# Optimization experiments

Measured on AMD Instinct MI355X. Metric: run time of the kernel, lower is better.

Reference implementation:

```python
import jax, jax.numpy as jnp
import numpy as np

N_NODES = 100000
N_EDGES = 6400000
D = 12

def setup_inputs() -> dict:
    key = jax.random.key(0)
    k1, k2, k3, k4 = jax.random.split(key, 4)
    x = jax.random.normal(k1, (N_NODES, D), dtype=jnp.float32)
    W_l = jax.random.normal(k2, (D, D), dtype=jnp.float32) / np.sqrt(D)
    W_r = jax.random.normal(k3, (D, D), dtype=jnp.float32) / np.sqrt(D)
    b = jnp.zeros((D,), dtype=jnp.float32)
    edge_index = jax.random.randint(k4, (2, N_EDGES), 0, N_NODES, dtype=jnp.int64)
    return {"x": x, "W_l": W_l, "W_r": W_r, "b": b, "edge_index": edge_index}

def reference(x, W_l, W_r, b, edge_index):
    # PyG SAGEConv (mean aggregation): out = lin_l(mean_{j in N(i)} x_j) + lin_r(x_i)
    src = edge_index[0]
    dst = edge_index[1]
    n = x.shape[0]
    msgs = x[src]                                      # [E, D] gather
    agg = jax.ops.segment_sum(msgs, dst, num_segments=n)          # [N, D]
    cnt = jax.ops.segment_sum(jnp.ones_like(dst, dtype=x.dtype), dst, num_segments=n)
    mean = agg / jnp.maximum(cnt, 1.0)[:, None]        # [N, D]
    out = mean @ W_l.T + x @ W_r.T + b                 # lin_l carries the bias in PyG
    return out
```

## Files before the change

kernel.cpp:

```cpp
#include <hip/hip_runtime.h>

#define N_NODES 100000
#define N_EDGES 6400000
#define D 12

#define SLOG 7
#define SSZ  128
#define NB   ((N_NODES + SSZ - 1) / SSZ)
#define NBLK 512
#define EPB  ((N_EDGES + NBLK - 1) / NBLK)
#define SBLK 256
#define STHR 512
#define SEPB ((N_EDGES + SBLK - 1) / SBLK)
#define RSTR 13

#define CAP  2048
#define EPT  (CAP / 256)

__device__ __forceinline__ unsigned int f2bf(float f) {
    unsigned int u = __float_as_uint(f);
    return (u + 0x7fffu + ((u >> 16) & 1u)) >> 16;
}
__device__ __forceinline__ unsigned int pk2(float lo, float hi) {
    return (f2bf(hi) << 16) | f2bf(lo);
}
__device__ __forceinline__ float bflo(unsigned int u) { return __uint_as_float(u << 16); }
__device__ __forceinline__ float bfhi(unsigned int u) { return __uint_as_float(u & 0xffff0000u); }

__global__ __launch_bounds__(256) void prep_kernel(
    const float* __restrict__ x, unsigned int* __restrict__ xb)
{
    int i = blockIdx.x * 256 + threadIdx.x;
    if (i >= N_NODES) return;
    const float4* xr = (const float4*)(x) + (size_t)i * 3;
    float4 a = xr[0], b = xr[1], c = xr[2];
    unsigned int* o = xb + (size_t)i * 8;
    ((uint4*)o)[0] = make_uint4(pk2(a.x, a.y), pk2(a.z, a.w), pk2(b.x, b.y), pk2(b.z, b.w));
    ((uint2*)(o + 4))[0] = make_uint2(pk2(c.x, c.y), pk2(c.z, c.w));
}

__global__ __launch_bounds__(256) void hist_kernel(
    const int* __restrict__ ei, int* __restrict__ bins)
{
    __shared__ int h[NB];
    for (int i = threadIdx.x; i < NB; i += 256) h[i] = 0;
    __syncthreads();
    const int* dei = ei + N_EDGES;
    int start = blockIdx.x * EPB;
    int end = min(start + EPB, N_EDGES);
    int e = start + (int)threadIdx.x;
    while (e + 768 < end) {
        int d0 = dei[e], d1 = dei[e + 256], d2 = dei[e + 512], d3 = dei[e + 768];
        atomicAdd(&h[d0 >> SLOG], 1);
        atomicAdd(&h[d1 >> SLOG], 1);
        atomicAdd(&h[d2 >> SLOG], 1);
        atomicAdd(&h[d3 >> SLOG], 1);
        e += 1024;
    }
    while (e < end) { atomicAdd(&h[dei[e] >> SLOG], 1); e += 256; }
    __syncthreads();
    for (int i = threadIdx.x; i < NB; i += 256) {
        int c = h[i];
        if (c) atomicAdd(&bins[i], c);
    }
}

__global__ __launch_bounds__(1024) void scan_kernel(
    const int* __restrict__ bins, int* __restrict__ base, int* __restrict__ cursor)
{
    __shared__ int buf[1024];
    __shared__ int carry;
    int tid = threadIdx.x;
    if (tid == 0) carry = 0;
    __syncthreads();
    for (int c0 = 0; c0 < NB; c0 += 1024) {
        int i = c0 + tid;
        int v = (i < NB) ? bins[i] : 0;
        buf[tid] = v;
        __syncthreads();
        for (int o = 1; o < 1024; o <<= 1) {
            int t = (tid >= o) ? buf[tid - o] : 0;
            __syncthreads();
            buf[tid] += t;
            __syncthreads();
        }
        int excl = buf[tid] - v + carry;
        if (i < NB) { base[i] = excl; cursor[i] = excl; }
        __syncthreads();
        if (tid == 0) carry += buf[1023];
        __syncthreads();
    }
    if (tid == 0) base[NB] = N_EDGES;
}

__global__ __launch_bounds__(512) void scatter_sort_kernel(
    const int* __restrict__ ei, int* __restrict__ cursor,
    unsigned int* __restrict__ sorted)
{
    __shared__ int h[NB];
    for (int i = threadIdx.x; i < NB; i += STHR) h[i] = 0;
    __syncthreads();
    const int* dei = ei + N_EDGES;
    int start = blockIdx.x * SEPB;
    int end = min(start + SEPB, N_EDGES);
    int e = start + (int)threadIdx.x;
    while (e + 3 * STHR < end) {
        int d0 = dei[e], d1 = dei[e + STHR], d2 = dei[e + 2 * STHR], d3 = dei[e + 3 * STHR];
        atomicAdd(&h[d0 >> SLOG], 1);
        atomicAdd(&h[d1 >> SLOG], 1);
        atomicAdd(&h[d2 >> SLOG], 1);
        atomicAdd(&h[d3 >> SLOG], 1);
        e += 4 * STHR;
    }
    while (e < end) { atomicAdd(&h[dei[e] >> SLOG], 1); e += STHR; }
    __syncthreads();
    for (int i = threadIdx.x; i < NB; i += STHR) {
        int c = h[i];
        h[i] = c ? atomicAdd(&cursor[i], c) : 0;
    }
    __syncthreads();
    e = start + (int)threadIdx.x;
    while (e + 3 * STHR < end) {
        int s0 = ei[e], s1 = ei[e + STHR], s2 = ei[e + 2 * STHR], s3 = ei[e + 3 * STHR];
        int d0 = dei[e], d1 = dei[e + STHR], d2 = dei[e + 2 * STHR], d3 = dei[e + 3 * STHR];
        int p0 = atomicAdd(&h[d0 >> SLOG], 1);
        int p1 = atomicAdd(&h[d1 >> SLOG], 1);
        int p2 = atomicAdd(&h[d2 >> SLOG], 1);
        int p3 = atomicAdd(&h[d3 >> SLOG], 1);
        sorted[p0] = ((unsigned)s0 << SLOG) | (unsigned)(d0 & (SSZ - 1));
        sorted[p1] = ((unsigned)s1 << SLOG) | (unsigned)(d1 & (SSZ - 1));
        sorted[p2] = ((unsigned)s2 << SLOG) | (unsigned)(d2 & (SSZ - 1));
        sorted[p3] = ((unsigned)s3 << SLOG) | (unsigned)(d3 & (SSZ - 1));
        e += 4 * STHR;
    }
    while (e < end) {
        int s = ei[e], d = dei[e];
        int pos = atomicAdd(&h[d >> SLOG], 1);
        sorted[pos] = ((unsigned)s << SLOG) | (unsigned)(d & (SSZ - 1));
        e += STHR;
    }
}

__global__ __launch_bounds__(256) void agg_reg_kernel(
    const unsigned int* __restrict__ sorted, const int* __restrict__ base,
    const unsigned int* __restrict__ xb,
    const float* __restrict__ x, const float* __restrict__ Wl,
    const float* __restrict__ Wr, const float* __restrict__ bias,
    float* __restrict__ out)
{
    __shared__ float sWl[D * D], sWr[D * D], sb[D];
    __shared__ int cnt[SSZ];
    __shared__ int sbuf[SSZ];
    __shared__ int segbase[SSZ + 1];
    __shared__ int cursor[SSZ];
    __shared__ int cnt_tot[SSZ];
    __shared__ unsigned vals[CAP * 6];

    int t = threadIdx.x;
    int b = blockIdx.x;

    if (t < D * D) { sWl[t] = Wl[t]; sWr[t] = Wr[t]; }
    if (t < D) sb[t] = bias[t];
    if (t < SSZ) cnt_tot[t] = 0;

    float acc[D];
#pragma unroll
    for (int d = 0; d < D; ++d) acc[d] = 0.f;

    int loc = t >> 1;
    int sub = t & 1;

    int start = base[b];
    int end = base[b + 1];

    for (int c0 = start; c0 < end; c0 += CAP) {
        int n = min(CAP, end - c0);
        if (t < SSZ) cnt[t] = 0;
        __syncthreads();

        unsigned pe[EPT];
        int ne = 0;
        for (int j = t; j < n; j += 256) pe[ne++] = sorted[c0 + j];
#pragma unroll
        for (int k = 0; k < EPT; ++k)
            if (k < ne) atomicAdd(&cnt[pe[k] & (SSZ - 1)], 1);
        __syncthreads();

        if (t < SSZ) sbuf[t] = cnt[t];
        __syncthreads();
        for (int o = 1; o < SSZ; o <<= 1) {
            int v = (t < SSZ && t >= o) ? sbuf[t - o] : 0;
            __syncthreads();
            if (t < SSZ) sbuf[t] += v;
            __syncthreads();
        }
        if (t < SSZ) {
            segbase[t + 1] = sbuf[t];
            if (t == 0) segbase[0] = 0;
        }
        __syncthreads();
        if (t < SSZ) { cursor[t] = segbase[t]; cnt_tot[t] += cnt[t]; }
        __syncthreads();

#pragma unroll
        for (int k = 0; k < EPT; ++k) {
            if (k < ne) {
                unsigned p = pe[k];
                int slot = atomicAdd(&cursor[p & (SSZ - 1)], 1);
                const unsigned* r = xb + (size_t)(p >> SLOG) * 8;
                uint2 q0 = ((const uint2*)r)[0];
                uint2 q1 = ((const uint2*)r)[1];
                uint2 q2 = ((const uint2*)r)[2];
                unsigned* vv = &vals[slot * 6];
                ((uint2*)vv)[0] = q0;
                ((uint2*)vv)[1] = q1;
                ((uint2*)vv)[2] = q2;
            }
        }
        __syncthreads();

        int s0 = segbase[loc], s1 = segbase[loc + 1];
        for (int j = s0 + sub; j < s1; j += 2) {
            const unsigned* vv = &vals[j * 6];
            uint2 q0 = ((const uint2*)vv)[0];
            uint2 q1 = ((const uint2*)vv)[1];
            uint2 q2 = ((const uint2*)vv)[2];
            acc[0]  += bflo(q0.x); acc[1]  += bfhi(q0.x);
            acc[2]  += bflo(q0.y); acc[3]  += bfhi(q0.y);
            acc[4]  += bflo(q1.x); acc[5]  += bfhi(q1.x);
            acc[6]  += bflo(q1.y); acc[7]  += bfhi(q1.y);
            acc[8]  += bflo(q2.x); acc[9]  += bfhi(q2.x);
            acc[10] += bflo(q2.y); acc[11] += bfhi(q2.y);
        }
        __syncthreads();
    }

    float* red = (float*)vals;
#pragma unroll
    for (int d = 0; d < D; ++d) red[sub * 1664 + loc * 13 + d] = acc[d];
    __syncthreads();

    if (t < SSZ) {
        int node = b * SSZ + t;
        if (node < N_NODES) {
            float m[D];
#pragma unroll
            for (int d = 0; d < D; ++d)
                m[d] = red[t * 13 + d] + red[1664 + t * 13 + d];
            float inv = 1.f / fmaxf((float)cnt_tot[t], 1.f);
#pragma unroll
            for (int d = 0; d < D; ++d) m[d] *= inv;

            float xi[D];
            const float4* xr = (const float4*)(x) + (size_t)node * 3;
            float4 x0 = xr[0], x1 = xr[1], x2 = xr[2];
            xi[0] = x0.x; xi[1] = x0.y; xi[2]  = x0.z; xi[3]  = x0.w;
            xi[4] = x1.x; xi[5] = x1.y; xi[6]  = x1.z; xi[7]  = x1.w;
            xi[8] = x2.x; xi[9] = x2.y; xi[10] = x2.z; xi[11] = x2.w;

            float o[D];
#pragma unroll
            for (int oo = 0; oo < D; ++oo) {
                float a = sb[oo];
#pragma unroll
                for (int d = 0; d < D; ++d) {
                    a += m[d] * sWl[oo * D + d];
                    a += xi[d] * sWr[oo * D + d];
                }
                o[oo] = a;
            }
            float4* orow = (float4*)(out) + (size_t)node * 3;
            orow[0] = make_float4(o[0], o[1], o[2], o[3]);
            orow[1] = make_float4(o[4], o[5], o[6], o[7]);
            orow[2] = make_float4(o[8], o[9], o[10], o[11]);
        }
    }
}

__global__ __launch_bounds__(256) void agg_finalize_f32_kernel(
    const unsigned int* __restrict__ sorted, const int* __restrict__ base,
    const float* __restrict__ x, const float* __restrict__ Wl,
    const float* __restrict__ Wr, const float* __restrict__ bias,
    float* __restrict__ out)
{
    __shared__ float agg[SSZ * RSTR];
    __shared__ float sWl[D * D], sWr[D * D], sb[D];
    int t = threadIdx.x;
    int b = blockIdx.x;
    for (int i = t; i < SSZ * RSTR; i += 256) agg[i] = 0.f;
    if (t < D * D) { sWl[t] = Wl[t]; sWr[t] = Wr[t]; }
    if (t < D) sb[t] = bias[t];
    __syncthreads();
    int start = base[b];
    int end = base[b + 1];
    for (int e = start + t; e < end; e += 256) {
        unsigned p = sorted[e];
        int src = (int)(p >> SLOG);
        int lc = (int)(p & (SSZ - 1));
        const float4* xr = (const float4*)(x) + (size_t)src * 3;
        float4 a = xr[0], b4 = xr[1], c = xr[2];
        float* ar = &agg[lc * RSTR];
        atomicAdd(ar + 0,  a.x);  atomicAdd(ar + 1,  a.y);
        atomicAdd(ar + 2,  a.z);  atomicAdd(ar + 3,  a.w);
        atomicAdd(ar + 4,  b4.x); atomicAdd(ar + 5,  b4.y);
        atomicAdd(ar + 6,  b4.z); atomicAdd(ar + 7,  b4.w);
        atomicAdd(ar + 8,  c.x);  atomicAdd(ar + 9,  c.y);
        atomicAdd(ar + 10, c.z);  atomicAdd(ar + 11, c.w);
        atomicAdd(ar + 12, 1.f);
    }
    __syncthreads();
    if (t < SSZ) {
        int node = b * SSZ + t;
        if (node < N_NODES) {
            const float* ar = &agg[t * RSTR];
            float inv = 1.f / fmaxf(ar[12], 1.f);
            float m[D], xi[D];
#pragma unroll
            for (int d = 0; d < D; ++d) m[d] = ar[d] * inv;
            const float4* xr = (const float4*)(x) + (size_t)node * 3;
            float4 x0 = xr[0], x1 = xr[1], x2 = xr[2];
            xi[0] = x0.x; xi[1] = x0.y; xi[2]  = x0.z; xi[3]  = x0.w;
            xi[4] = x1.x; xi[5] = x1.y; xi[6]  = x1.z; xi[7]  = x1.w;
            xi[8] = x2.x; xi[9] = x2.y; xi[10] = x2.z; xi[11] = x2.w;
            float o[D];
#pragma unroll
            for (int oo = 0; oo < D; ++oo) {
                float a = sb[oo];
#pragma unroll
                for (int d = 0; d < D; ++d) {
                    a += m[d] * sWl[oo * D + d];
                    a += xi[d] * sWr[oo * D + d];
                }
                o[oo] = a;
            }
            float4* orow = (float4*)(out) + (size_t)node * 3;
            orow[0] = make_float4(o[0], o[1], o[2], o[3]);
            orow[1] = make_float4(o[4], o[5], o[6], o[7]);
            orow[2] = make_float4(o[8], o[9], o[10], o[11]);
        }
    }
}


__global__ __launch_bounds__(256) void scatter_kernel(
    const int* __restrict__ ei, const float* __restrict__ x,
    float* __restrict__ agg, float* __restrict__ cnt)
{
    int e = blockIdx.x * blockDim.x + threadIdx.x;
    if (e >= N_EDGES) return;
    int src = ei[e];
    int dst = ei[N_EDGES + e];
    const float4* xr = (const float4*)(x + (size_t)src * D);
    float4 a = xr[0], b4 = xr[1], c = xr[2];
    float* dr = agg + (size_t)dst * D;
    atomicAdd(dr + 0,  a.x);  atomicAdd(dr + 1,  a.y);
    atomicAdd(dr + 2,  a.z);  atomicAdd(dr + 3,  a.w);
    atomicAdd(dr + 4,  b4.x); atomicAdd(dr + 5,  b4.y);
    atomicAdd(dr + 6,  b4.z); atomicAdd(dr + 7,  b4.w);
    atomicAdd(dr + 8,  c.x);  atomicAdd(dr + 9,  c.y);
    atomicAdd(dr + 10, c.z);  atomicAdd(dr + 11, c.w);
    atomicAdd(cnt + dst, 1.0f);
}

__global__ __launch_bounds__(256) void finalize_kernel(
    const float* __restrict__ x, const float* __restrict__ Wl,
    const float* __restrict__ Wr, const float* __restrict__ bias,
    const float* __restrict__ agg, const float* __restrict__ cnt,
    float* __restrict__ out)
{
    __shared__ float sWl[D * D], sWr[D * D], sb[D];
    int t = threadIdx.x;
    if (t < D * D) { sWl[t] = Wl[t]; sWr[t] = Wr[t]; }
    if (t < D) sb[t] = bias[t];
    __syncthreads();
    int i = blockIdx.x * blockDim.x + t;
    if (i >= N_NODES) return;
    float inv = 1.0f / fmaxf(cnt[i], 1.0f);
    float m[D], xi[D];
    const float4* ar = (const float4*)(agg + (size_t)i * D);
    const float4* xr = (const float4*)(x + (size_t)i * D);
    float4 a0 = ar[0], a1 = ar[1], a2 = ar[2];
    float4 x0 = xr[0], x1 = xr[1], x2 = xr[2];
    m[0] = a0.x * inv; m[1] = a0.y * inv; m[2]  = a0.z * inv; m[3]  = a0.w * inv;
    m[4] = a1.x * inv; m[5] = a1.y * inv; m[6]  = a1.z * inv; m[7]  = a1.w * inv;
    m[8] = a2.x * inv; m[9] = a2.y * inv; m[10] = a2.z * inv; m[11] = a2.w * inv;
    xi[0] = x0.x; xi[1] = x0.y; xi[2]  = x0.z; xi[3]  = x0.w;
    xi[4] = x1.x; xi[5] = x1.y; xi[6]  = x1.z; xi[7]  = x1.w;
    xi[8] = x2.x; xi[9] = x2.y; xi[10] = x2.z; xi[11] = x2.w;
    float o[D];
#pragma unroll
    for (int oo = 0; oo < D; ++oo) {
        float acc = sb[oo];
#pragma unroll
        for (int d = 0; d < D; ++d) {
            acc += m[d] * sWl[oo * D + d];
            acc += xi[d] * sWr[oo * D + d];
        }
        o[oo] = acc;
    }
    float4* orow = (float4*)(out + (size_t)i * D);
    orow[0] = make_float4(o[0], o[1], o[2], o[3]);
    orow[1] = make_float4(o[4], o[5], o[6], o[7]);
    orow[2] = make_float4(o[8], o[9], o[10], o[11]);
}

extern "C" void kernel_launch(void* const* d_in, const int* in_sizes, int n_in,
                              void* d_out, int out_size, void* d_ws, size_t ws_size,
                              hipStream_t stream) {
    const float* x    = (const float*)d_in[0];
    const float* Wl   = (const float*)d_in[1];
    const float* Wr   = (const float*)d_in[2];
    const float* bias = (const float*)d_in[3];
    const int*   ei   = (const int*)d_in[4];
    float* out = (float*)d_out;

    size_t sortedBytes = (size_t)N_EDGES * sizeof(unsigned int);
    size_t xbBytes     = (size_t)N_NODES * 8 * sizeof(unsigned int);
    size_t binsBytes   = (size_t)NB * sizeof(int);
    size_t baseBytes   = (size_t)(NB + 1) * sizeof(int);
    size_t neededFull = sortedBytes + xbBytes + binsBytes + baseBytes + binsBytes;
    size_t neededMid  = sortedBytes + binsBytes + baseBytes + binsBytes;
    size_t neededLast = ((size_t)N_NODES * D + N_NODES) * sizeof(float);

    if (ws_size >= neededFull) {
        char* p = (char*)d_ws;
        unsigned int* sorted = (unsigned int*)p;        p += sortedBytes;
        unsigned int* xb     = (unsigned int*)p;        p += xbBytes;
        int* bins   = (int*)p;                          p += binsBytes;
        int* base   = (int*)p;                          p += baseBytes;
        int* cursor = (int*)p;

        hipMemsetAsync(bins, 0, binsBytes, stream);
        prep_kernel<<<(N_NODES + 255) / 256, 256, 0, stream>>>(x, xb);
        hist_kernel<<<NBLK, 256, 0, stream>>>(ei, bins);
        scan_kernel<<<1, 1024, 0, stream>>>(bins, base, cursor);
        scatter_sort_kernel<<<SBLK, STHR, 0, stream>>>(ei, cursor, sorted);
        agg_reg_kernel<<<NB, 256, 0, stream>>>(sorted, base, xb, x, Wl, Wr, bias, out);
    } else if (ws_size >= neededMid) {
        char* p = (char*)d_ws;
        unsigned int* sorted = (unsigned int*)p;        p += sortedBytes;
        int* bins   = (int*)p;                          p += binsBytes;
        int* base   = (int*)p;                          p += baseBytes;
        int* cursor = (int*)p;

        hipMemsetAsync(bins, 0, binsBytes, stream);
        hist_kernel<<<NBLK, 256, 0, stream>>>(ei, bins);
        scan_kernel<<<1, 1024, 0, stream>>>(bins, base, cursor);
        scatter_sort_kernel<<<SBLK, STHR, 0, stream>>>(ei, cursor, sorted);
        agg_finalize_f32_kernel<<<NB, 256, 0, stream>>>(sorted, base, x, Wl, Wr, bias, out);
    } else {
        float* agg = (float*)d_ws;
        float* cnt = agg + (size_t)N_NODES * D;
        hipMemsetAsync(d_ws, 0, neededLast, stream);
        scatter_kernel<<<(N_EDGES + 255) / 256, 256, 0, stream>>>(ei, x, agg, cnt);
        finalize_kernel<<<(N_NODES + 255) / 256, 256, 0, stream>>>(x, Wl, Wr, bias, agg, cnt, out);
    }
}
```

Baseline: 271.8 us.

## Replace global-atomic bucket sort with per-block histogram counting and scan

Splits the edge bucket sort into a per-block count pass, a single-block scan that computes global bucket bases and per-block write offsets, and a placement pass. This removes the duplicate histogram pass in the scatter kernel, the memset and the global atomic cursor claims. It also adds nontemporal loads for the streamed edge and sorted arrays. The cost is a larger workspace and a serial single-workgroup scan over all per-block counts, which may become a latency bottleneck.

New measurement: 295.9 us. +8.8%, slower.

```diff
diff --git a/kernel.cpp b/kernel.cpp
--- a/kernel.cpp
+++ b/kernel.cpp
@@ -7,11 +7,9 @@
 #define SLOG 7
 #define SSZ  128
 #define NB   ((N_NODES + SSZ - 1) / SSZ)
-#define NBLK 512
-#define EPB  ((N_EDGES + NBLK - 1) / NBLK)
 #define SBLK 256
 #define STHR 512
-#define SEPB ((N_EDGES + SBLK - 1) / SBLK)
+#define SEPB (N_EDGES / SBLK)
 #define RSTR 13
 
 #define CAP  2048
@@ -39,90 +37,106 @@
     ((uint2*)(o + 4))[0] = make_uint2(pk2(c.x, c.y), pk2(c.z, c.w));
 }
 
-__global__ __launch_bounds__(256) void hist_kernel(
-    const int* __restrict__ ei, int* __restrict__ bins)
+__global__ __launch_bounds__(512) void count_kernel(
+    const int* __restrict__ ei, int* __restrict__ cnt)
 {
     __shared__ int h[NB];
-    for (int i = threadIdx.x; i < NB; i += 256) h[i] = 0;
-    __syncthreads();
-    const int* dei = ei + N_EDGES;
-    int start = blockIdx.x * EPB;
-    int end = min(start + EPB, N_EDGES);
-    int e = start + (int)threadIdx.x;
-    while (e + 768 < end) {
-        int d0 = dei[e], d1 = dei[e + 256], d2 = dei[e + 512], d3 = dei[e + 768];
-        atomicAdd(&h[d0 >> SLOG], 1);
-        atomicAdd(&h[d1 >> SLOG], 1);
-        atomicAdd(&h[d2 >> SLOG], 1);
-        atomicAdd(&h[d3 >> SLOG], 1);
-        e += 1024;
-    }
-    while (e < end) { atomicAdd(&h[dei[e] >> SLOG], 1); e += 256; }
-    __syncthreads();
-    for (int i = threadIdx.x; i < NB; i += 256) {
-        int c = h[i];
-        if (c) atomicAdd(&bins[i], c);
-    }
-}
-
-__global__ __launch_bounds__(1024) void scan_kernel(
-    const int* __restrict__ bins, int* __restrict__ base, int* __restrict__ cursor)
-{
-    __shared__ int buf[1024];
-    __shared__ int carry;
-    int tid = threadIdx.x;
-    if (tid == 0) carry = 0;
-    __syncthreads();
-    for (int c0 = 0; c0 < NB; c0 += 1024) {
-        int i = c0 + tid;
-        int v = (i < NB) ? bins[i] : 0;
-        buf[tid] = v;
-        __syncthreads();
-        for (int o = 1; o < 1024; o <<= 1) {
-            int t = (tid >= o) ? buf[tid - o] : 0;
-            __syncthreads();
-            buf[tid] += t;
-            __syncthreads();
-        }
-        int excl = buf[tid] - v + carry;
-        if (i < NB) { base[i] = excl; cursor[i] = excl; }
-        __syncthreads();
-        if (tid == 0) carry += buf[1023];
-        __syncthreads();
-    }
-    if (tid == 0) base[NB] = N_EDGES;
-}
-
-__global__ __launch_bounds__(512) void scatter_sort_kernel(
-    const int* __restrict__ ei, int* __restrict__ cursor,
-    unsigned int* __restrict__ sorted)
-{
-    __shared__ int h[NB];
-    for (int i = threadIdx.x; i < NB; i += STHR) h[i] = 0;
+    int t = threadIdx.x;
+    for (int i = t; i < NB; i += STHR) h[i] = 0;
     __syncthreads();
     const int* dei = ei + N_EDGES;
     int start = blockIdx.x * SEPB;
-    int end = min(start + SEPB, N_EDGES);
-    int e = start + (int)threadIdx.x;
+    int end = start + SEPB;
+    int e = start + t;
     while (e + 3 * STHR < end) {
-        int d0 = dei[e], d1 = dei[e + STHR], d2 = dei[e + 2 * STHR], d3 = dei[e + 3 * STHR];
+        int d0 = __builtin_nontemporal_load(&dei[e]);
+        int d1 = __builtin_nontemporal_load(&dei[e + STHR]);
+        int d2 = __builtin_nontemporal_load(&dei[e + 2 * STHR]);
+        int d3 = __builtin_nontemporal_load(&dei[e + 3 * STHR]);
         atomicAdd(&h[d0 >> SLOG], 1);
         atomicAdd(&h[d1 >> SLOG], 1);
         atomicAdd(&h[d2 >> SLOG], 1);
         atomicAdd(&h[d3 >> SLOG], 1);
         e += 4 * STHR;
     }
-    while (e < end) { atomicAdd(&h[dei[e] >> SLOG], 1); e += STHR; }
-    __syncthreads();
-    for (int i = threadIdx.x; i < NB; i += STHR) {
-        int c = h[i];
-        h[i] = c ? atomicAdd(&cursor[i], c) : 0;
-    }
-    __syncthreads();
-    e = start + (int)threadIdx.x;
+    while (e < end) {
+        int d = __builtin_nontemporal_load(&dei[e]);
+        atomicAdd(&h[d >> SLOG], 1);
+        e += STHR;
+    }
+    __syncthreads();
+    int* row = cnt + (size_t)blockIdx.x * NB;
+    for (int i = t; i < NB; i += STHR) row[i] = h[i];
+}
+
+__global__ __launch_bounds__(1024) void scan2_kernel(
+    const int* __restrict__ cnt, int* __restrict__ base, int* __restrict__ blockcur)
+{
+    __shared__ int buf[1024];
+    int tid = threadIdx.x;
+    int tot = 0;
+    if (tid < NB) {
+        int s0 = 0, s1 = 0, s2 = 0, s3 = 0, s4 = 0, s5 = 0, s6 = 0, s7 = 0;
+        for (int b = 0; b < SBLK; b += 8) {
+            s0 += cnt[(size_t)(b + 0) * NB + tid];
+            s1 += cnt[(size_t)(b + 1) * NB + tid];
+            s2 += cnt[(size_t)(b + 2) * NB + tid];
+            s3 += cnt[(size_t)(b + 3) * NB + tid];
+            s4 += cnt[(size_t)(b + 4) * NB + tid];
+            s5 += cnt[(size_t)(b + 5) * NB + tid];
+            s6 += cnt[(size_t)(b + 6) * NB + tid];
+            s7 += cnt[(size_t)(b + 7) * NB + tid];
+        }
+        tot = ((s0 + s1) + (s2 + s3)) + ((s4 + s5) + (s6 + s7));
+    }
+    buf[tid] = (tid < NB) ? tot : 0;
+    __syncthreads();
+    for (int o = 1; o < 1024; o <<= 1) {
+        int v = (tid >= o) ? buf[tid - o] : 0;
+        __syncthreads();
+        buf[tid] += v;
+        __syncthreads();
+    }
+    int excl = buf[tid] - tot;
+    if (tid < NB) base[tid] = excl;
+    if (tid == 0) base[NB] = N_EDGES;
+    if (tid < NB) {
+        int run = excl;
+        for (int b0 = 0; b0 < SBLK; b0 += 8) {
+            int c[8];
+#pragma unroll
+            for (int i = 0; i < 8; ++i) c[i] = cnt[(size_t)(b0 + i) * NB + tid];
+#pragma unroll
+            for (int i = 0; i < 8; ++i) {
+                blockcur[(size_t)(b0 + i) * NB + tid] = run;
+                run += c[i];
+            }
+        }
+    }
+}
+
+__global__ __launch_bounds__(512) void place_kernel(
+    const int* __restrict__ ei, const int* __restrict__ blockcur,
+    unsigned int* __restrict__ sorted)
+{
+    __shared__ int h[NB];
+    int t = threadIdx.x;
+    const int* row = blockcur + (size_t)blockIdx.x * NB;
+    for (int i = t; i < NB; i += STHR) h[i] = row[i];
+    __syncthreads();
+    const int* dei = ei + N_EDGES;
+    int start = blockIdx.x * SEPB;
+    int end = start + SEPB;
+    int e = start + t;
     while (e + 3 * STHR < end) {
-        int s0 = ei[e], s1 = ei[e + STHR], s2 = ei[e + 2 * STHR], s3 = ei[e + 3 * STHR];
-        int d0 = dei[e], d1 = dei[e + STHR], d2 = dei[e + 2 * STHR], d3 = dei[e + 3 * STHR];
+        int s0 = __builtin_nontemporal_load(&ei[e]);
+        int s1 = __builtin_nontemporal_load(&ei[e + STHR]);
+        int s2 = __builtin_nontemporal_load(&ei[e + 2 * STHR]);
+        int s3 = __builtin_nontemporal_load(&ei[e + 3 * STHR]);
+        int d0 = __builtin_nontemporal_load(&dei[e]);
+        int d1 = __builtin_nontemporal_load(&dei[e + STHR]);
+        int d2 = __builtin_nontemporal_load(&dei[e + 2 * STHR]);
+        int d3 = __builtin_nontemporal_load(&dei[e + 3 * STHR]);
         int p0 = atomicAdd(&h[d0 >> SLOG], 1);
         int p1 = atomicAdd(&h[d1 >> SLOG], 1);
         int p2 = atomicAdd(&h[d2 >> SLOG], 1);
@@ -134,7 +148,8 @@
         e += 4 * STHR;
     }
     while (e < end) {
-        int s = ei[e], d = dei[e];
+        int s = __builtin_nontemporal_load(&ei[e]);
+        int d = __builtin_nontemporal_load(&dei[e]);
         int pos = atomicAdd(&h[d >> SLOG], 1);
         sorted[pos] = ((unsigned)s << SLOG) | (unsigned)(d & (SSZ - 1));
         e += STHR;
@@ -180,7 +195,7 @@
 
         unsigned pe[EPT];
         int ne = 0;
-        for (int j = t; j < n; j += 256) pe[ne++] = sorted[c0 + j];
+        for (int j = t; j < n; j += 256) pe[ne++] = __builtin_nontemporal_load(&sorted[c0 + j]);
 #pragma unroll
         for (int k = 0; k < EPT; ++k)
             if (k < ne) atomicAdd(&cnt[pe[k] & (SSZ - 1)], 1);
@@ -414,39 +429,38 @@
     const int*   ei   = (const int*)d_in[4];
     float* out = (float*)d_out;
 
-    size_t sortedBytes = (size_t)N_EDGES * sizeof(unsigned int);
-    size_t xbBytes     = (size_t)N_NODES * 8 * sizeof(unsigned int);
-    size_t binsBytes   = (size_t)NB * sizeof(int);
-    size_t baseBytes   = (size_t)(NB + 1) * sizeof(int);
-    size_t neededFull = sortedBytes + xbBytes + binsBytes + baseBytes + binsBytes;
-    size_t neededMid  = sortedBytes + binsBytes + baseBytes + binsBytes;
+    size_t sortedBytes   = (size_t)N_EDGES * sizeof(unsigned int);
+    size_t xbBytes       = (size_t)N_NODES * 8 * sizeof(unsigned int);
+    size_t cntBytes      = (size_t)SBLK * NB * sizeof(int);
+    size_t blockcurBytes = cntBytes;
+    size_t baseBytes     = (size_t)(NB + 1) * sizeof(int);
+    size_t neededFull = sortedBytes + xbBytes + cntBytes + blockcurBytes + baseBytes;
+    size_t neededMid  = sortedBytes + cntBytes + blockcurBytes + baseBytes;
     size_t neededLast = ((size_t)N_NODES * D + N_NODES) * sizeof(float);
 
     if (ws_size >= neededFull) {
         char* p = (char*)d_ws;
         unsigned int* sorted = (unsigned int*)p;        p += sortedBytes;
         unsigned int* xb     = (unsigned int*)p;        p += xbBytes;
-        int* bins   = (int*)p;                          p += binsBytes;
-        int* base   = (int*)p;                          p += baseBytes;
-        int* cursor = (int*)p;
-
-        hipMemsetAsync(bins, 0, binsBytes, stream);
+        int* cnt      = (int*)p;                        p += cntBytes;
+        int* blockcur = (int*)p;                        p += blockcurBytes;
+        int* base     = (int*)p;
+
         prep_kernel<<<(N_NODES + 255) / 256, 256, 0, stream>>>(x, xb);
-        hist_kernel<<<NBLK, 256, 0, stream>>>(ei, bins);
-        scan_kernel<<<1, 1024, 0, stream>>>(bins, base, cursor);
-        scatter_sort_kernel<<<SBLK, STHR, 0, stream>>>(ei, cursor, sorted);
+        count_kernel<<<SBLK, STHR, 0, stream>>>(ei, cnt);
+        scan2_kernel<<<1, 1024, 0, stream>>>(cnt, base, blockcur);
+        place_kernel<<<SBLK, STHR, 0, stream>>>(ei, blockcur, sorted);
         agg_reg_kernel<<<NB, 256, 0, stream>>>(sorted, base, xb, x, Wl, Wr, bias, out);
     } else if (ws_size >= neededMid) {
         char* p = (char*)d_ws;
         unsigned int* sorted = (unsigned int*)p;        p += sortedBytes;
-        int* bins   = (int*)p;                          p += binsBytes;
-        int* base   = (int*)p;                          p += baseBytes;
-        int* cursor = (int*)p;
-
-        hipMemsetAsync(bins, 0, binsBytes, stream);
-        hist_kernel<<<NBLK, 256, 0, stream>>>(ei, bins);
-        scan_kernel<<<1, 1024, 0, stream>>>(bins, base, cursor);
-        scatter_sort_kernel<<<SBLK, STHR, 0, stream>>>(ei, cursor, sorted);
+        int* cnt      = (int*)p;                        p += cntBytes;
+        int* blockcur = (int*)p;                        p += blockcurBytes;
+        int* base     = (int*)p;
+
+        count_kernel<<<SBLK, STHR, 0, stream>>>(ei, cnt);
+        scan2_kernel<<<1, 1024, 0, stream>>>(cnt, base, blockcur);
+        place_kernel<<<SBLK, STHR, 0, stream>>>(ei, blockcur, sorted);
         agg_finalize_f32_kernel<<<NB, 256, 0, stream>>>(sorted, base, x, Wl, Wr, bias, out);
     } else {
         float* agg = (float*)d_ws;
```

## Replace global histogram+scan+scatter with per-block local partition and segmented gather

Applied to the files above, without the earlier changes.

Merges the histogram, single-block scan and scatter kernels into one partition kernel. Each block sorts its own contiguous edge slice by destination bucket into a private region and writes per-bucket counts and offsets. The aggregation kernel then gathers each bucket's edges from all 256 per-block segments, using a prefix sum and a binary search per edge. This removes the memset, the global atomics on the cursor array and the serial scan launch. In exchange it adds a 256-wide scan and binary-search indexing per edge in the aggregation kernel, and reads of a per-block, per-bucket count matrix. CAP is reduced and the middle fallback path is dropped.

Result: slower. 287.3 us (+5.7%).

```diff
diff --git a/kernel.cpp b/kernel.cpp
--- a/kernel.cpp
+++ b/kernel.cpp
@@ -7,14 +7,12 @@
 #define SLOG 7
 #define SSZ  128
 #define NB   ((N_NODES + SSZ - 1) / SSZ)
-#define NBLK 512
-#define EPB  ((N_EDGES + NBLK - 1) / NBLK)
 #define SBLK 256
 #define STHR 512
-#define SEPB ((N_EDGES + SBLK - 1) / SBLK)
+#define SEPB (N_EDGES / SBLK)
 #define RSTR 13
 
-#define CAP  2048
+#define CAP  1792
 #define EPT  (CAP / 256)
 
 __device__ __forceinline__ unsigned int f2bf(float f) {
@@ -39,71 +37,23 @@
     ((uint2*)(o + 4))[0] = make_uint2(pk2(c.x, c.y), pk2(c.z, c.w));
 }
 
-__global__ __launch_bounds__(256) void hist_kernel(
-    const int* __restrict__ ei, int* __restrict__ bins)
+__global__ __launch_bounds__(512) void part_kernel(
+    const int* __restrict__ ei, int* __restrict__ cnt, int* __restrict__ rowpre,
+    unsigned int* __restrict__ sorted)
 {
     __shared__ int h[NB];
-    for (int i = threadIdx.x; i < NB; i += 256) h[i] = 0;
-    __syncthreads();
+    __shared__ int cur[NB];
+    __shared__ int sb2[512];
+    int t = threadIdx.x;
+    int b = blockIdx.x;
+    for (int i = t; i < NB; i += STHR) h[i] = 0;
+    __syncthreads();
+
     const int* dei = ei + N_EDGES;
-    int start = blockIdx.x * EPB;
-    int end = min(start + EPB, N_EDGES);
-    int e = start + (int)threadIdx.x;
-    while (e + 768 < end) {
-        int d0 = dei[e], d1 = dei[e + 256], d2 = dei[e + 512], d3 = dei[e + 768];
-        atomicAdd(&h[d0 >> SLOG], 1);
-        atomicAdd(&h[d1 >> SLOG], 1);
-        atomicAdd(&h[d2 >> SLOG], 1);
-        atomicAdd(&h[d3 >> SLOG], 1);
-        e += 1024;
-    }
-    while (e < end) { atomicAdd(&h[dei[e] >> SLOG], 1); e += 256; }
-    __syncthreads();
-    for (int i = threadIdx.x; i < NB; i += 256) {
-        int c = h[i];
-        if (c) atomicAdd(&bins[i], c);
-    }
-}
-
-__global__ __launch_bounds__(1024) void scan_kernel(
-    const int* __restrict__ bins, int* __restrict__ base, int* __restrict__ cursor)
-{
-    __shared__ int buf[1024];
-    __shared__ int carry;
-    int tid = threadIdx.x;
-    if (tid == 0) carry = 0;
-    __syncthreads();
-    for (int c0 = 0; c0 < NB; c0 += 1024) {
-        int i = c0 + tid;
-        int v = (i < NB) ? bins[i] : 0;
-        buf[tid] = v;
-        __syncthreads();
-        for (int o = 1; o < 1024; o <<= 1) {
-            int t = (tid >= o) ? buf[tid - o] : 0;
-            __syncthreads();
-            buf[tid] += t;
-            __syncthreads();
-        }
-        int excl = buf[tid] - v + carry;
-        if (i < NB) { base[i] = excl; cursor[i] = excl; }
-        __syncthreads();
-        if (tid == 0) carry += buf[1023];
-        __syncthreads();
-    }
-    if (tid == 0) base[NB] = N_EDGES;
-}
-
-__global__ __launch_bounds__(512) void scatter_sort_kernel(
-    const int* __restrict__ ei, int* __restrict__ cursor,
-    unsigned int* __restrict__ sorted)
-{
-    __shared__ int h[NB];
-    for (int i = threadIdx.x; i < NB; i += STHR) h[i] = 0;
-    __syncthreads();
-    const int* dei = ei + N_EDGES;
-    int start = blockIdx.x * SEPB;
-    int end = min(start + SEPB, N_EDGES);
-    int e = start + (int)threadIdx.x;
+    int start = b * SEPB;
+    int end = start + SEPB;
+
+    int e = start + t;
     while (e + 3 * STHR < end) {
         int d0 = dei[e], d1 = dei[e + STHR], d2 = dei[e + 2 * STHR], d3 = dei[e + 3 * STHR];
         atomicAdd(&h[d0 >> SLOG], 1);
@@ -114,36 +64,59 @@
     }
     while (e < end) { atomicAdd(&h[dei[e] >> SLOG], 1); e += STHR; }
     __syncthreads();
-    for (int i = threadIdx.x; i < NB; i += STHR) {
-        int c = h[i];
-        h[i] = c ? atomicAdd(&cursor[i], c) : 0;
-    }
-    __syncthreads();
-    e = start + (int)threadIdx.x;
+
+    int* crow = cnt + (size_t)b * NB;
+    for (int i = t; i < NB; i += STHR) crow[i] = h[i];
+
+    int pairv = 0;
+    if (t < (NB + 1) / 2) {
+        pairv = h[2 * t] + ((2 * t + 1 < NB) ? h[2 * t + 1] : 0);
+    }
+    sb2[t] = pairv;
+    __syncthreads();
+    for (int o = 1; o < 512; o <<= 1) {
+        int v = (t >= o) ? sb2[t - o] : 0;
+        __syncthreads();
+        sb2[t] += v;
+        __syncthreads();
+    }
+    if (t < (NB + 1) / 2) {
+        int excl = sb2[t] - pairv;
+        cur[2 * t] = excl;
+        if (2 * t + 1 < NB) cur[2 * t + 1] = excl + h[2 * t];
+    }
+    __syncthreads();
+
+    int* rrow = rowpre + (size_t)b * NB;
+    for (int i = t; i < NB; i += STHR) rrow[i] = cur[i];
+    __syncthreads();
+
+    unsigned int* dst = sorted + (size_t)b * SEPB;
+    e = start + t;
     while (e + 3 * STHR < end) {
         int s0 = ei[e], s1 = ei[e + STHR], s2 = ei[e + 2 * STHR], s3 = ei[e + 3 * STHR];
         int d0 = dei[e], d1 = dei[e + STHR], d2 = dei[e + 2 * STHR], d3 = dei[e + 3 * STHR];
-        int p0 = atomicAdd(&h[d0 >> SLOG], 1);
-        int p1 = atomicAdd(&h[d1 >> SLOG], 1);
-        int p2 = atomicAdd(&h[d2 >> SLOG], 1);
-        int p3 = atomicAdd(&h[d3 >> SLOG], 1);
-        sorted[p0] = ((unsigned)s0 << SLOG) | (unsigned)(d0 & (SSZ - 1));
-        sorted[p1] = ((unsigned)s1 << SLOG) | (unsigned)(d1 & (SSZ - 1));
-        sorted[p2] = ((unsigned)s2 << SLOG) | (unsigned)(d2 & (SSZ - 1));
-        sorted[p3] = ((unsigned)s3 << SLOG) | (unsigned)(d3 & (SSZ - 1));
+        int p0 = atomicAdd(&cur[d0 >> SLOG], 1);
+        int p1 = atomicAdd(&cur[d1 >> SLOG], 1);
+        int p2 = atomicAdd(&cur[d2 >> SLOG], 1);
+        int p3 = atomicAdd(&cur[d3 >> SLOG], 1);
+        dst[p0] = ((unsigned)s0 << SLOG) | (unsigned)(d0 & (SSZ - 1));
+        dst[p1] = ((unsigned)s1 << SLOG) | (unsigned)(d1 & (SSZ - 1));
+        dst[p2] = ((unsigned)s2 << SLOG) | (unsigned)(d2 & (SSZ - 1));
+        dst[p3] = ((unsigned)s3 << SLOG) | (unsigned)(d3 & (SSZ - 1));
         e += 4 * STHR;
     }
     while (e < end) {
         int s = ei[e], d = dei[e];
-        int pos = atomicAdd(&h[d >> SLOG], 1);
-        sorted[pos] = ((unsigned)s << SLOG) | (unsigned)(d & (SSZ - 1));
+        int pos = atomicAdd(&cur[d >> SLOG], 1);
+        dst[pos] = ((unsigned)s << SLOG) | (unsigned)(d & (SSZ - 1));
         e += STHR;
     }
 }
 
 __global__ __launch_bounds__(256) void agg_reg_kernel(
-    const unsigned int* __restrict__ sorted, const int* __restrict__ base,
-    const unsigned int* __restrict__ xb,
+    const unsigned int* __restrict__ sorted, const int* __restrict__ cntm,
+    const int* __restrict__ rowpre, const unsigned int* __restrict__ xb,
     const float* __restrict__ x, const float* __restrict__ Wl,
     const float* __restrict__ Wr, const float* __restrict__ bias,
     float* __restrict__ out)
@@ -154,15 +127,39 @@
     __shared__ int segbase[SSZ + 1];
     __shared__ int cursor[SSZ];
     __shared__ int cnt_tot[SSZ];
+    __shared__ int seglen[SBLK];
+    __shared__ int segoff[SBLK];
+    __shared__ int segpre[SBLK + 1];
     __shared__ unsigned vals[CAP * 6];
 
     int t = threadIdx.x;
-    int b = blockIdx.x;
+    int k = blockIdx.x;
 
     if (t < D * D) { sWl[t] = Wl[t]; sWr[t] = Wr[t]; }
     if (t < D) sb[t] = bias[t];
     if (t < SSZ) cnt_tot[t] = 0;
 
+    if (t < SBLK) {
+        seglen[t] = cntm[(size_t)t * NB + k];
+        segoff[t] = t * SEPB + rowpre[(size_t)t * NB + k];
+    }
+    __syncthreads();
+    int sl = (t < SBLK) ? seglen[t] : 0;
+    if (t < SBLK) sbuf[0] = 0;
+    {
+        if (t < SBLK) segpre[t + 1] = sl;
+        if (t == 0) segpre[0] = 0;
+        __syncthreads();
+        for (int o = 1; o < SBLK; o <<= 1) {
+            int v = 0;
+            if (t < SBLK && (int)t + 1 > o) v = segpre[t + 1 - o];
+            __syncthreads();
+            if (t < SBLK) segpre[t + 1] += v;
+            __syncthreads();
+        }
+    }
+    int T = segpre[SBLK];
+
     float acc[D];
 #pragma unroll
     for (int d = 0; d < D; ++d) acc[d] = 0.f;
@@ -170,20 +167,26 @@
     int loc = t >> 1;
     int sub = t & 1;
 
-    int start = base[b];
-    int end = base[b + 1];
-
-    for (int c0 = start; c0 < end; c0 += CAP) {
-        int n = min(CAP, end - c0);
+    for (int c0 = 0; c0 < T; c0 += CAP) {
+        int n = min(CAP, T - c0);
         if (t < SSZ) cnt[t] = 0;
         __syncthreads();
 
         unsigned pe[EPT];
         int ne = 0;
-        for (int j = t; j < n; j += 256) pe[ne++] = sorted[c0 + j];
-#pragma unroll
-        for (int k = 0; k < EPT; ++k)
-            if (k < ne) atomicAdd(&cnt[pe[k] & (SSZ - 1)], 1);
+        for (int j = t; j < n; j += 256) {
+            int v = c0 + j;
+            int lo = 0, hi = SBLK;
+            while (hi - lo > 1) {
+                int mid = (lo + hi) >> 1;
+                if (segpre[mid] <= v) lo = mid; else hi = mid;
+            }
+            int gi = segoff[lo] + (v - segpre[lo]);
+            pe[ne++] = sorted[gi];
+        }
+#pragma unroll
+        for (int q = 0; q < EPT; ++q)
+            if (q < ne) atomicAdd(&cnt[pe[q] & (SSZ - 1)], 1);
         __syncthreads();
 
         if (t < SSZ) sbuf[t] = cnt[t];
@@ -203,9 +206,9 @@
         __syncthreads();
 
 #pragma unroll
-        for (int k = 0; k < EPT; ++k) {
-            if (k < ne) {
-                unsigned p = pe[k];
+        for (int q = 0; q < EPT; ++q) {
+            if (q < ne) {
+                unsigned p = pe[q];
                 int slot = atomicAdd(&cursor[p & (SSZ - 1)], 1);
                 const unsigned* r = xb + (size_t)(p >> SLOG) * 8;
                 uint2 q0 = ((const uint2*)r)[0];
@@ -241,7 +244,7 @@
     __syncthreads();
 
     if (t < SSZ) {
-        int node = b * SSZ + t;
+        int node = k * SSZ + t;
         if (node < N_NODES) {
             float m[D];
 #pragma unroll
@@ -258,70 +261,6 @@
             xi[4] = x1.x; xi[5] = x1.y; xi[6]  = x1.z; xi[7]  = x1.w;
             xi[8] = x2.x; xi[9] = x2.y; xi[10] = x2.z; xi[11] = x2.w;
 
-            float o[D];
-#pragma unroll
-            for (int oo = 0; oo < D; ++oo) {
-                float a = sb[oo];
-#pragma unroll
-                for (int d = 0; d < D; ++d) {
-                    a += m[d] * sWl[oo * D + d];
-                    a += xi[d] * sWr[oo * D + d];
-                }
-                o[oo] = a;
-            }
-            float4* orow = (float4*)(out) + (size_t)node * 3;
-            orow[0] = make_float4(o[0], o[1], o[2], o[3]);
-            orow[1] = make_float4(o[4], o[5], o[6], o[7]);
-            orow[2] = make_float4(o[8], o[9], o[10], o[11]);
-        }
-    }
-}
-
-__global__ __launch_bounds__(256) void agg_finalize_f32_kernel(
-    const unsigned int* __restrict__ sorted, const int* __restrict__ base,
-    const float* __restrict__ x, const float* __restrict__ Wl,
-    const float* __restrict__ Wr, const float* __restrict__ bias,
-    float* __restrict__ out)
-{
-    __shared__ float agg[SSZ * RSTR];
-    __shared__ float sWl[D * D], sWr[D * D], sb[D];
-    int t = threadIdx.x;
-    int b = blockIdx.x;
-    for (int i = t; i < SSZ * RSTR; i += 256) agg[i] = 0.f;
-    if (t < D * D) { sWl[t] = Wl[t]; sWr[t] = Wr[t]; }
-    if (t < D) sb[t] = bias[t];
-    __syncthreads();
-    int start = base[b];
-    int end = base[b + 1];
-    for (int e = start + t; e < end; e += 256) {
-        unsigned p = sorted[e];
-        int src = (int)(p >> SLOG);
-        int lc = (int)(p & (SSZ - 1));
-        const float4* xr = (const float4*)(x) + (size_t)src * 3;
-        float4 a = xr[0], b4 = xr[1], c = xr[2];
-        float* ar = &agg[lc * RSTR];
-        atomicAdd(ar + 0,  a.x);  atomicAdd(ar + 1,  a.y);
-        atomicAdd(ar + 2,  a.z);  atomicAdd(ar + 3,  a.w);
-        atomicAdd(ar + 4,  b4.x); atomicAdd(ar + 5,  b4.y);
-        atomicAdd(ar + 6,  b4.z); atomicAdd(ar + 7,  b4.w);
-        atomicAdd(ar + 8,  c.x);  atomicAdd(ar + 9,  c.y);
-        atomicAdd(ar + 10, c.z);  atomicAdd(ar + 11, c.w);
-        atomicAdd(ar + 12, 1.f);
-    }
-    __syncthreads();
-    if (t < SSZ) {
-        int node = b * SSZ + t;
-        if (node < N_NODES) {
-            const float* ar = &agg[t * RSTR];
-            float inv = 1.f / fmaxf(ar[12], 1.f);
-            float m[D], xi[D];
-#pragma unroll
-            for (int d = 0; d < D; ++d) m[d] = ar[d] * inv;
-            const float4* xr = (const float4*)(x) + (size_t)node * 3;
-            float4 x0 = xr[0], x1 = xr[1], x2 = xr[2];
-            xi[0] = x0.x; xi[1] = x0.y; xi[2]  = x0.z; xi[3]  = x0.w;
-            xi[4] = x1.x; xi[5] = x1.y; xi[6]  = x1.z; xi[7]  = x1.w;
-            xi[8] = x2.x; xi[9] = x2.y; xi[10] = x2.z; xi[11] = x2.w;
             float o[D];
 #pragma unroll
             for (int oo = 0; oo < D; ++oo) {
@@ -416,38 +355,21 @@
 
     size_t sortedBytes = (size_t)N_EDGES * sizeof(unsigned int);
     size_t xbBytes     = (size_t)N_NODES * 8 * sizeof(unsigned int);
-    size_t binsBytes   = (size_t)NB * sizeof(int);
-    size_t baseBytes   = (size_t)(NB + 1) * sizeof(int);
-    size_t neededFull = sortedBytes + xbBytes + binsBytes + baseBytes + binsBytes;
-    size_t neededMid  = sortedBytes + binsBytes + baseBytes + binsBytes;
+    size_t cntBytes    = (size_t)SBLK * NB * sizeof(int);
+    size_t rowpreBytes = cntBytes;
+    size_t neededFull = sortedBytes + xbBytes + cntBytes + rowpreBytes;
     size_t neededLast = ((size_t)N_NODES * D + N_NODES) * sizeof(float);
 
     if (ws_size >= neededFull) {
         char* p = (char*)d_ws;
         unsigned int* sorted = (unsigned int*)p;        p += sortedBytes;
         unsigned int* xb     = (unsigned int*)p;        p += xbBytes;
-        int* bins   = (int*)p;                          p += binsBytes;
-        int* base   = (int*)p;                          p += baseBytes;
-        int* cursor = (int*)p;
-
-        hipMemsetAsync(bins, 0, binsBytes, stream);
+        int* cnt    = (int*)p;                          p += cntBytes;
+        int* rowpre = (int*)p;
+
         prep_kernel<<<(N_NODES + 255) / 256, 256, 0, stream>>>(x, xb);
-        hist_kernel<<<NBLK, 256, 0, stream>>>(ei, bins);
-        scan_kernel<<<1, 1024, 0, stream>>>(bins, base, cursor);
-        scatter_sort_kernel<<<SBLK, STHR, 0, stream>>>(ei, cursor, sorted);
-        agg_reg_kernel<<<NB, 256, 0, stream>>>(sorted, base, xb, x, Wl, Wr, bias, out);
-    } else if (ws_size >= neededMid) {
-        char* p = (char*)d_ws;
-        unsigned int* sorted = (unsigned int*)p;        p += sortedBytes;
-        int* bins   = (int*)p;                          p += binsBytes;
-        int* base   = (int*)p;                          p += baseBytes;
-        int* cursor = (int*)p;
-
-        hipMemsetAsync(bins, 0, binsBytes, stream);
-        hist_kernel<<<NBLK, 256, 0, stream>>>(ei, bins);
-        scan_kernel<<<1, 1024, 0, stream>>>(bins, base, cursor);
-        scatter_sort_kernel<<<SBLK, STHR, 0, stream>>>(ei, cursor, sorted);
-        agg_finalize_f32_kernel<<<NB, 256, 0, stream>>>(sorted, base, x, Wl, Wr, bias, out);
+        part_kernel<<<SBLK, STHR, 0, stream>>>(ei, cnt, rowpre, sorted);
+        agg_reg_kernel<<<NB, 256, 0, stream>>>(sorted, cnt, rowpre, xb, x, Wl, Wr, bias, out);
     } else {
         float* agg = (float*)d_ws;
         float* cnt = agg + (size_t)N_NODES * D;
```
